# Performance work log

Measured on AMD Instinct MI355X. Metric: run time of the kernel, lower is better.

## Reference

```python
import jax, jax.numpy as jnp
import numpy as np

S, D, M, K, H = 4096, 768, 1024, 32, 8
DH = D // H  # 96
CTX = 10
EPS_LN = 1e-5
EPS_COS = 1e-8


def setup_inputs() -> dict:
    key = jax.random.key(0)
    ks = jax.random.split(key, 30)
    sc = 0.02
    n = lambda k, shp: jax.random.normal(k, shp, jnp.float32) * sc
    inp = {
        "text_embeddings": jax.random.normal(ks[0], (1, S, D), jnp.float32),
        "candidate_embeddings": jax.random.normal(ks[1], (M, K, D), jnp.float32),
        "mention_starts": jax.random.randint(ks[2], (M,), 0, S - 16),
        "span_lengths": jax.random.randint(ks[3], (M,), 0, 8),
        # relik_reader: Linear(2D->D), ReLU, Linear(D->1)
        "relik_w1": n(ks[4], (2 * D, D)), "relik_b1": jnp.zeros((D,), jnp.float32),
        "relik_w2": n(ks[5], (D, 1)), "relik_b2": jnp.zeros((1,), jnp.float32),
        # TransformerEncoderLayer (post-norm, relu, nhead=8, ffn=4D)
        "wq": n(ks[6], (D, D)), "bq": jnp.zeros((D,), jnp.float32),
        "wk": n(ks[7], (D, D)), "bk": jnp.zeros((D,), jnp.float32),
        "wv": n(ks[8], (D, D)), "bv": jnp.zeros((D,), jnp.float32),
        "wo": n(ks[9], (D, D)), "bo": jnp.zeros((D,), jnp.float32),
        "ln1_g": jnp.ones((D,), jnp.float32), "ln1_b": jnp.zeros((D,), jnp.float32),
        "ffn_w1": n(ks[10], (D, 4 * D)), "ffn_b1": jnp.zeros((4 * D,), jnp.float32),
        "ffn_w2": n(ks[11], (4 * D, D)), "ffn_b2": jnp.zeros((D,), jnp.float32),
        "ln2_g": jnp.ones((D,), jnp.float32), "ln2_b": jnp.zeros((D,), jnp.float32),
        # unirel_interaction: Linear(2D->D), ReLU, Linear(D->D)
        "uni_w1": n(ks[12], (2 * D, D)), "uni_b1": jnp.zeros((D,), jnp.float32),
        "uni_w2": n(ks[13], (D, D)), "uni_b2": jnp.zeros((D,), jnp.float32),
    }
    return inp


def _ln(x, g, b):
    mu = jnp.mean(x, -1, keepdims=True)
    var = jnp.mean(jnp.square(x - mu), -1, keepdims=True)
    return (x - mu) * jax.lax.rsqrt(var + EPS_LN) * g + b


def reference(text_embeddings, candidate_embeddings, mention_starts, span_lengths,
              relik_w1, relik_b1, relik_w2, relik_b2,
              wq, bq, wk, bk, wv, bv, wo, bo,
              ln1_g, ln1_b, ffn_w1, ffn_b1, ffn_w2, ffn_b2, ln2_g, ln2_b,
              uni_w1, uni_b1, uni_w2, uni_b2):
    txt = text_embeddings[0]                               # [S, D]
    seq = txt.shape[0]
    csum = jnp.concatenate([jnp.zeros((1, txt.shape[1]), txt.dtype),
                            jnp.cumsum(txt, axis=0)], axis=0)  # [S+1, D]
    ends = mention_starts + span_lengths
    # mean over [start, end] inclusive
    m_len = (span_lengths + 1).astype(txt.dtype)
    mention = (csum[ends + 1] - csum[mention_starts]) / m_len[:, None]  # [M, D]
    # context mean over [c_start, c_end) exclusive, as in original slicing
    c_start = jnp.maximum(0, mention_starts - CTX)
    c_end = jnp.minimum(seq - 1, ends + CTX)
    ctx = (csum[c_end] - csum[c_start]) / (c_end - c_start).astype(txt.dtype)[:, None]

    cand = candidate_embeddings                            # [M, K, D]
    mk = jnp.broadcast_to(mention[:, None, :], cand.shape) # [M, K, D]

    # relik score: MLP on [mention; candidate]
    cat_mc = jnp.concatenate([mk, cand], axis=-1)          # [M, K, 2D]
    h = jax.nn.relu(cat_mc @ relik_w1 + relik_b1)
    relik = (h @ relik_w2 + relik_b2)[..., 0]              # [M, K]

    # 2-token transformer encoder layer over stack([mention, candidate])
    x = jnp.stack([mk, cand], axis=2)                      # [M, K, 2, D]
    q = (x @ wq + bq).reshape(M, K, 2, H, DH)
    k_ = (x @ wk + bk).reshape(M, K, 2, H, DH)
    v = (x @ wv + bv).reshape(M, K, 2, H, DH)
    scores = jnp.einsum("mkqhd,mkvhd->mkhqv", q, k_) / jnp.sqrt(jnp.float32(DH))
    attn = jax.nn.softmax(scores, axis=-1)
    o = jnp.einsum("mkhqv,mkvhd->mkqhd", attn, v).reshape(M, K, 2, D)
    x1 = _ln(x + (o @ wo + bo), ln1_g, ln1_b)
    f = jax.nn.relu(x1 @ ffn_w1 + ffn_b1) @ ffn_w2 + ffn_b2
    x2 = _ln(x1 + f, ln2_g, ln2_b)                         # [M, K, 2, D]
    e0, e1 = x2[..., 0, :], x2[..., 1, :]
    n0 = jnp.maximum(jnp.linalg.norm(e0, axis=-1), EPS_COS)
    n1 = jnp.maximum(jnp.linalg.norm(e1, axis=-1), EPS_COS)
    atg = jnp.sum(e0 * e1, axis=-1) / (n0 * n1)            # [M, K]

    # unirel: MLP on [context; candidate], sigmoid of mean
    ck = jnp.broadcast_to(ctx[:, None, :], cand.shape)
    cat_cc = jnp.concatenate([ck, cand], axis=-1)
    inter = jax.nn.relu(cat_cc @ uni_w1 + uni_b1) @ uni_w2 + uni_b2
    unirel = jax.nn.sigmoid(jnp.mean(inter, axis=-1))      # [M, K]

    return jnp.stack([relik, atg, unirel], axis=0)         # [3, M, K]
```

## Files before the change

### kernel.cpp

```cpp
#include <hip/hip_runtime.h>
#include <math.h>

#define S_LEN 4096
#define D_DIM 768
#define M_CNT 1024
#define K_CNT 32
#define MK_CNT 32768
#define DH_DIM 96
#define CTX_W 10

typedef __bf16 bf16_t;
typedef bf16_t bf16x8 __attribute__((ext_vector_type(8)));
typedef float f32x4 __attribute__((ext_vector_type(4)));
typedef float f32x16 __attribute__((ext_vector_type(16)));
typedef int i32x4 __attribute__((ext_vector_type(4)));
typedef int i32x8 __attribute__((ext_vector_type(8)));

__device__ __forceinline__ float block_reduce_sum(float v, float* sbuf) {
#pragma unroll
    for (int off = 32; off; off >>= 1) v += __shfl_down(v, off);
    __syncthreads();
    int wave = threadIdx.x >> 6;
    int lane = threadIdx.x & 63;
    if (lane == 0) sbuf[wave] = v;
    __syncthreads();
    return sbuf[0] + sbuf[1] + sbuf[2] + sbuf[3];
}

__device__ __forceinline__ float wave_sum(float v) {
#pragma unroll
    for (int off = 32; off; off >>= 1) v += __shfl_down(v, off);
    return __shfl(v, 0);
}

__device__ __forceinline__ unsigned char to_fp8(float v) {
    return (unsigned char)(__builtin_amdgcn_cvt_pk_fp8_f32(v, v, 0, false) & 0xff);
}

__device__ __forceinline__ void ld2(const bf16_t* p, float& a, float& b) {
    ushort2 u = *(const ushort2*)p;
    a = __uint_as_float((unsigned)u.x << 16);
    b = __uint_as_float((unsigned)u.y << 16);
}

template<int OUT_BF16, int RELU>
__global__ __launch_bounds__(256, 2) void gemm_mfma(
    const bf16_t* __restrict__ A, const bf16_t* __restrict__ Bt,
    const float* __restrict__ bias, void* __restrict__ C,
    int Kd, int N, int nx, int ny)
{
    __shared__ bf16_t As[128 * 64];
    __shared__ bf16_t Bs[128 * 64];
    const int tid = threadIdx.x;
    const int w = tid >> 6, l = tid & 63;
    int per = 8 * nx;
    int g = blockIdx.x / per, rr = blockIdx.x % per;
    int gs = ny - g * 8; if (gs > 8) gs = 8;
    const int row0 = (g * 8 + rr % gs) * 128, col0 = (rr / gs) * 128;

    const int srow = w * 8 + (l >> 3);
    const int gchunk = (l & 7) ^ ((l >> 3) & 7);
    const bf16_t* gA = A + (size_t)(row0 + srow) * Kd + gchunk * 8;
    const bf16_t* gB = Bt + (size_t)(col0 + srow) * Kd + gchunk * 8;

    const int wm = w >> 1, wn = w & 1;
    f32x4 acc[4][4] = {};

    for (int k0 = 0; k0 < Kd; k0 += 64) {
#pragma unroll
        for (int c = 0; c < 4; ++c) {
            __builtin_amdgcn_global_load_lds(
                (const __attribute__((address_space(1))) void*)(gA + (size_t)(c * 32) * Kd + k0),
                (__attribute__((address_space(3))) void*)(As + (c * 256 + w * 64) * 8), 16, 0, 0);
            __builtin_amdgcn_global_load_lds(
                (const __attribute__((address_space(1))) void*)(gB + (size_t)(c * 32) * Kd + k0),
                (__attribute__((address_space(3))) void*)(Bs + (c * 256 + w * 64) * 8), 16, 0, 0);
        }
        __syncthreads();
#pragma unroll
        for (int ks = 0; ks < 2; ++ks) {
            bf16x8 af[4], bfr[4];
#pragma unroll
            for (int i = 0; i < 4; ++i) {
                int arow = wm * 64 + i * 16 + (l & 15);
                int slot = (ks * 4 + (l >> 4)) ^ (l & 7);
                af[i] = *(const bf16x8*)(As + arow * 64 + slot * 8);
                int brow = wn * 64 + i * 16 + (l & 15);
                bfr[i] = *(const bf16x8*)(Bs + brow * 64 + slot * 8);
            }
#pragma unroll
            for (int i = 0; i < 4; ++i)
#pragma unroll
                for (int j = 0; j < 4; ++j)
                    acc[i][j] = __builtin_amdgcn_mfma_f32_16x16x32_bf16(af[i], bfr[j], acc[i][j], 0, 0, 0);
        }
        __syncthreads();
    }

#pragma unroll
    for (int i = 0; i < 4; ++i) {
        int row = row0 + wm * 64 + i * 16 + (l >> 4) * 4;
#pragma unroll
        for (int j = 0; j < 4; ++j) {
            int col = col0 + wn * 64 + j * 16 + (l & 15);
            float bv = bias ? bias[col] : 0.f;
#pragma unroll
            for (int r = 0; r < 4; ++r) {
                float v = acc[i][j][r] + bv;
                if (RELU) v = fmaxf(v, 0.f);
                if (OUT_BF16) ((bf16_t*)C)[(size_t)(row + r) * N + col] = (bf16_t)v;
                else          ((float*)C)[(size_t)(row + r) * N + col] = v;
            }
        }
    }
}

static inline void launch_gemm(const bf16_t* A, const bf16_t* Bt, const float* bias, void* C,
                               int rows, int Kd, int N, bool relu, bool outbf, hipStream_t st) {
    int nx = N / 128, ny = rows / 128;
    dim3 grid(nx * ny);
    if (outbf) {
        if (relu) gemm_mfma<1, 1><<<grid, 256, 0, st>>>(A, Bt, bias, C, Kd, N, nx, ny);
        else      gemm_mfma<1, 0><<<grid, 256, 0, st>>>(A, Bt, bias, C, Kd, N, nx, ny);
    } else {
        if (relu) gemm_mfma<0, 1><<<grid, 256, 0, st>>>(A, Bt, bias, C, Kd, N, nx, ny);
        else      gemm_mfma<0, 0><<<grid, 256, 0, st>>>(A, Bt, bias, C, Kd, N, nx, ny);
    }
}

template<int OMODE, int RELU, int RESID>
__global__ __launch_bounds__(256, 2) void gemm_fp8(
    const unsigned char* __restrict__ A, const unsigned char* __restrict__ Bp,
    const float* __restrict__ bias, void* __restrict__ C,
    const bf16_t* __restrict__ resid,
    int Kd, int N, int nx, int ny)
{
    __shared__ unsigned char As[256 * 128];
    const int tid = threadIdx.x;
    const int w = tid >> 6, l = tid & 63;
    int per = 8 * nx;
    int g = blockIdx.x / per, rrb = blockIdx.x % per;
    int gs = ny - g * 8; if (gs > 8) gs = 8;
    const int row0 = (g * 8 + rrb % gs) * 256, col0 = (rrb / gs) * 128;
    const int wm = w >> 1, wn = w & 1;
    const int SA = 0x7F7F7F7F;
    const int KT = Kd >> 7;

    const int srow = w * 8 + (l >> 3);
    const int gch = (l & 7) ^ ((l >> 3) & 7);
    const unsigned char* gA = A + (size_t)(row0 + srow) * Kd + gch * 16;

    const int cg0 = (col0 >> 5) + wn * 2;
    const unsigned char* gB0 = Bp + (size_t)cg0 * KT * 4096 + (l >> 5) * 1024 + (l & 31) * 16;
    const unsigned char* gB1 = gB0 + (size_t)KT * 4096;

    f32x16 acc[4][2] = {};

    for (int kt = 0; kt < KT; ++kt) {
#pragma unroll
        for (int q = 0; q < 8; ++q)
            __builtin_amdgcn_global_load_lds(
                (const __attribute__((address_space(1))) void*)(gA + (size_t)(q * 32) * Kd + kt * 128),
                (__attribute__((address_space(3))) void*)(As + (q * 256 + w * 64) * 16), 16, 0, 0);

        const unsigned char* p0 = gB0 + (size_t)kt * 4096;
        const unsigned char* p1 = gB1 + (size_t)kt * 4096;
        i32x4 b00l = *(const i32x4*)(p0);
        i32x4 b00h = *(const i32x4*)(p0 + 512);
        i32x4 b01l = *(const i32x4*)(p0 + 2048);
        i32x4 b01h = *(const i32x4*)(p0 + 2560);
        i32x4 b10l = *(const i32x4*)(p1);
        i32x4 b10h = *(const i32x4*)(p1 + 512);
        i32x4 b11l = *(const i32x4*)(p1 + 2048);
        i32x4 b11h = *(const i32x4*)(p1 + 2560);

        __syncthreads();

#pragma unroll
        for (int s = 0; s < 2; ++s) {
            int cb = s * 4 + ((l >> 5) << 1);
            i32x8 af[4], bfr[2];
#pragma unroll
            for (int i = 0; i < 4; ++i) {
                int row = wm * 128 + i * 32 + (l & 31);
                int sl0 = cb ^ (row & 7);
                int sl1 = (cb + 1) ^ (row & 7);
                i32x4 lo = *(const i32x4*)(As + (row * 8 + sl0) * 16);
                i32x4 hi = *(const i32x4*)(As + (row * 8 + sl1) * 16);
                i32x8 a;
                a[0] = lo[0]; a[1] = lo[1]; a[2] = lo[2]; a[3] = lo[3];
                a[4] = hi[0]; a[5] = hi[1]; a[6] = hi[2]; a[7] = hi[3];
                af[i] = a;
            }
            {
                i32x4 lo = s ? b01l : b00l;
                i32x4 hi = s ? b01h : b00h;
                i32x8 b;
                b[0] = lo[0]; b[1] = lo[1]; b[2] = lo[2]; b[3] = lo[3];
                b[4] = hi[0]; b[5] = hi[1]; b[6] = hi[2]; b[7] = hi[3];
                bfr[0] = b;
                lo = s ? b11l : b10l;
                hi = s ? b11h : b10h;
                b[0] = lo[0]; b[1] = lo[1]; b[2] = lo[2]; b[3] = lo[3];
                b[4] = hi[0]; b[5] = hi[1]; b[6] = hi[2]; b[7] = hi[3];
                bfr[1] = b;
            }
#pragma unroll
            for (int i = 0; i < 4; ++i)
#pragma unroll
                for (int j = 0; j < 2; ++j)
                    acc[i][j] = __builtin_amdgcn_mfma_scale_f32_32x32x64_f8f6f4(
                        af[i], bfr[j], acc[i][j], 0, 0, 0, SA, 0, SA);
        }
        __syncthreads();
    }

#pragma unroll
    for (int i = 0; i < 4; ++i) {
        int rbase = row0 + wm * 128 + i * 32 + 4 * (l >> 5);
#pragma unroll
        for (int j = 0; j < 2; ++j) {
            int col = col0 + wn * 64 + j * 32 + (l & 31);
            float bv = bias ? bias[col] : 0.f;
#pragma unroll
            for (int reg = 0; reg < 16; ++reg) {
                int row = rbase + (reg & 3) + 8 * (reg >> 2);
                float v = acc[i][j][reg] + bv;
                if (RESID) v += (float)resid[(size_t)row * N + col];
                if (RELU) v = fmaxf(v, 0.f);
                if (OMODE == 1)
                    ((unsigned char*)C)[(size_t)row * N + col] = to_fp8(v);
                else if (OMODE == 2)
                    ((bf16_t*)C)[(size_t)row * N + col] = (bf16_t)v;
                else
                    ((float*)C)[(size_t)row * N + col] = v;
            }
        }
    }
}

template<int OMODE, int RELU, int RESID>
static inline void launch_fp8_t(const unsigned char* A, const unsigned char* Bp, const float* bias,
                                void* C, const bf16_t* resid, int rows, int Kd, int N, hipStream_t st) {
    int nx = N / 128, ny = rows / 256;
    gemm_fp8<OMODE, RELU, RESID><<<dim3(nx * ny), 256, 0, st>>>(A, Bp, bias, C, resid, Kd, N, nx, ny);
}

__global__ __launch_bounds__(256) void transpose_bf16(
    const float* __restrict__ W, bf16_t* __restrict__ Wt, int Kd, int N)
{
    __shared__ float t[32][33];
    int bx = blockIdx.x * 32, by = blockIdx.y * 32;
    int x = threadIdx.x & 31, y = threadIdx.x >> 5;
#pragma unroll
    for (int yy = y; yy < 32; yy += 8) t[yy][x] = W[(size_t)(by + yy) * N + bx + x];
    __syncthreads();
#pragma unroll
    for (int yy = y; yy < 32; yy += 8) Wt[(size_t)(bx + yy) * Kd + by + x] = (bf16_t)t[x][yy];
}

__global__ __launch_bounds__(256) void pack_fp8(
    const float* __restrict__ W, unsigned char* __restrict__ P, int Kd, int N)
{
    __shared__ float t[32][33];
    int bx = blockIdx.x * 32, by = blockIdx.y * 32;
    int x = threadIdx.x & 31, y = threadIdx.x >> 5;
#pragma unroll
    for (int yy = y; yy < 32; yy += 8) t[yy][x] = W[(size_t)(by + yy) * N + bx + x];
    __syncthreads();
    int xg = threadIdx.x & 7, yo = threadIdx.x >> 3;
    int lo = __builtin_amdgcn_cvt_pk_fp8_f32(t[xg * 4 + 0][yo], t[xg * 4 + 1][yo], 0, false);
    int both = __builtin_amdgcn_cvt_pk_fp8_f32(t[xg * 4 + 2][yo], t[xg * 4 + 3][yo], lo, true);
    int cg = blockIdx.x;
    int kt = by >> 7;
    int s = (by >> 6) & 1;
    int half = (by >> 5) & 1;
    int chunk = xg >> 2;
    size_t off = (((size_t)cg * (Kd >> 7) + kt) * 4096) + s * 2048 + half * 1024
               + chunk * 512 + yo * 16 + (xg & 3) * 4;
    *(int*)(P + off) = both;
}

__global__ __launch_bounds__(256) void cvt_cand(
    const float* __restrict__ x, bf16_t* __restrict__ yb,
    unsigned char* __restrict__ yq, int n4)
{
    int i = blockIdx.x * 256 + threadIdx.x;
    if (i < n4) {
        float4 v = ((const float4*)x)[i];
        bf16_t o4[4] = {(bf16_t)v.x, (bf16_t)v.y, (bf16_t)v.z, (bf16_t)v.w};
        ((uint2*)yb)[i] = *(uint2*)o4;
        int lo = __builtin_amdgcn_cvt_pk_fp8_f32(v.x, v.y, 0, false);
        int both = __builtin_amdgcn_cvt_pk_fp8_f32(v.z, v.w, lo, true);
        ((int*)yq)[i] = both;
    }
}

__global__ __launch_bounds__(256) void pack_bias(
    const float* __restrict__ bq, const float* __restrict__ bk,
    const float* __restrict__ bv, float* __restrict__ o)
{
    int i = blockIdx.x * 256 + threadIdx.x;
    if (i < 768) { o[i] = bq[i]; o[i + 768] = bk[i]; o[i + 1536] = bv[i]; }
}

__global__ __launch_bounds__(256) void spans_kernel(
    const float* __restrict__ txt, const int* __restrict__ starts,
    const int* __restrict__ lens, float* __restrict__ mention,
    unsigned char* __restrict__ mentionq, bf16_t* __restrict__ mentionb,
    bf16_t* __restrict__ ctxb)
{
    int m = blockIdx.x;
    int st = starts[m], ln = lens[m];
    int en = st + ln;
    int cs = st - CTX_W; if (cs < 0) cs = 0;
    int ce = en + CTX_W; if (ce > S_LEN - 1) ce = S_LEN - 1;
    int c = threadIdx.x;
    float s0 = 0.f, s1 = 0.f, s2 = 0.f;
    for (int r = st; r <= en; ++r) {
        const float* tr = txt + (size_t)r * D_DIM;
        s0 += tr[c]; s1 += tr[c + 256]; s2 += tr[c + 512];
    }
    float inv = 1.f / (float)(ln + 1);
    float v0 = s0 * inv, v1 = s1 * inv, v2 = s2 * inv;
    float* mp = mention + (size_t)m * D_DIM;
    bf16_t* mb = mentionb + (size_t)m * D_DIM;
    unsigned char* mq = mentionq + (size_t)m * D_DIM;
    mp[c] = v0; mp[c + 256] = v1; mp[c + 512] = v2;
    mb[c] = (bf16_t)v0; mb[c + 256] = (bf16_t)v1; mb[c + 512] = (bf16_t)v2;
    mq[c] = to_fp8(v0); mq[c + 256] = to_fp8(v1); mq[c + 512] = to_fp8(v2);

    s0 = 0.f; s1 = 0.f; s2 = 0.f;
    for (int r = cs; r < ce; ++r) {
        const float* tr = txt + (size_t)r * D_DIM;
        s0 += tr[c]; s1 += tr[c + 256]; s2 += tr[c + 512];
    }
    inv = 1.f / (float)(ce - cs);
    bf16_t* cp = ctxb + (size_t)m * D_DIM;
    cp[c] = (bf16_t)(s0 * inv); cp[c + 256] = (bf16_t)(s1 * inv); cp[c + 512] = (bf16_t)(s2 * inv);
}

__global__ __launch_bounds__(256) void w2bar_kernel(
    const float* __restrict__ uni_w2, const float* __restrict__ uni_b2,
    float* __restrict__ w2bar, float* __restrict__ b2bar)
{
    __shared__ float sbuf[4];
    int d = blockIdx.x;
    float s = 0.f;
    if (d < D_DIM) {
        for (int j = threadIdx.x; j < D_DIM; j += 256) s += uni_w2[(size_t)d * D_DIM + j];
        s = block_reduce_sum(s, sbuf);
        if (threadIdx.x == 0) w2bar[d] = s * (1.f / (float)D_DIM);
    } else {
        for (int j = threadIdx.x; j < D_DIM; j += 256) s += uni_b2[j];
        s = block_reduce_sum(s, sbuf);
        if (threadIdx.x == 0) *b2bar = s * (1.f / (float)D_DIM);
    }
}

__global__ __launch_bounds__(512) void attn_kernel(
    const bf16_t* __restrict__ qkvm, const bf16_t* __restrict__ qkvc,
    unsigned char* __restrict__ o, int g0)
{
    int lc = blockIdx.x;
    int gg = g0 + lc;
    int m = gg >> 5;
    int h = threadIdx.x >> 6;
    int lane = threadIdx.x & 63;
    const bf16_t* bm = qkvm + (size_t)m * 2304 + h * DH_DIM;
    const bf16_t* bc = qkvc + (size_t)lc * 2304 + h * DH_DIM;

    float s00 = 0.f, s01 = 0.f, s10 = 0.f, s11 = 0.f;
    int d = lane * 2;
    if (lane < 48) {
        float qm0, qm1, km0, km1, qc0, qc1, kc0, kc1;
        ld2(bm + d, qm0, qm1);
        ld2(bm + 768 + d, km0, km1);
        ld2(bc + d, qc0, qc1);
        ld2(bc + 768 + d, kc0, kc1);
        s00 = qm0 * km0 + qm1 * km1;
        s01 = qm0 * kc0 + qm1 * kc1;
        s10 = qc0 * km0 + qc1 * km1;
        s11 = qc0 * kc0 + qc1 * kc1;
    }
#pragma unroll
    for (int off = 32; off; off >>= 1) {
        s00 += __shfl_down(s00, off); s01 += __shfl_down(s01, off);
        s10 += __shfl_down(s10, off); s11 += __shfl_down(s11, off);
    }
    s00 = __shfl(s00, 0); s01 = __shfl(s01, 0);
    s10 = __shfl(s10, 0); s11 = __shfl(s11, 0);
    const float sc = 0.1020620726159658f;
    s00 *= sc; s01 *= sc; s10 *= sc; s11 *= sc;
    float m0 = fmaxf(s00, s01), m1 = fmaxf(s10, s11);
    float e00 = expf(s00 - m0), e01 = expf(s01 - m0);
    float e10 = expf(s10 - m1), e11 = expf(s11 - m1);
    float i0 = 1.f / (e00 + e01), i1 = 1.f / (e10 + e11);
    float a00 = e00 * i0, a01 = e01 * i0, a10 = e10 * i1, a11 = e11 * i1;

    unsigned char* o0 = o + ((size_t)lc * 2) * D_DIM + h * DH_DIM;
    unsigned char* o1 = o0 + D_DIM;
    if (lane < 48) {
        float vm0, vm1, vc0, vc1;
        ld2(bm + 1536 + d, vm0, vm1);
        ld2(bc + 1536 + d, vc0, vc1);
        unsigned r0 = __builtin_amdgcn_cvt_pk_fp8_f32(a00 * vm0 + a01 * vc0, a00 * vm1 + a01 * vc1, 0, false);
        unsigned r1 = __builtin_amdgcn_cvt_pk_fp8_f32(a10 * vm0 + a11 * vc0, a10 * vm1 + a11 * vc1, 0, false);
        *(unsigned short*)(o0 + d) = (unsigned short)(r0 & 0xffff);
        *(unsigned short*)(o1 + d) = (unsigned short)(r1 & 0xffff);
    }
}

__global__ __launch_bounds__(256) void ln1_kernel(
    const bf16_t* __restrict__ x1pre, const float* __restrict__ mention,
    const bf16_t* __restrict__ candb, const float* __restrict__ g,
    const float* __restrict__ b, bf16_t* __restrict__ x1f,
    unsigned char* __restrict__ x1q, int g0)
{
    int w = threadIdx.x >> 6, l = threadIdx.x & 63;
    int r = blockIdx.x * 4 + w;
    int lc = r >> 1, pos = r & 1;
    int gg = g0 + lc, m = gg >> 5;
    float v[12];
    const bf16_t* pr = x1pre + (size_t)r * D_DIM;
    if (pos) {
        const bf16_t* xr = candb + (size_t)gg * D_DIM;
#pragma unroll
        for (int i = 0; i < 12; ++i) { int j = l + i * 64; v[i] = (float)xr[j] + (float)pr[j]; }
    } else {
        const float* xr = mention + (size_t)m * D_DIM;
#pragma unroll
        for (int i = 0; i < 12; ++i) { int j = l + i * 64; v[i] = xr[j] + (float)pr[j]; }
    }
    float s = 0.f;
#pragma unroll
    for (int i = 0; i < 12; ++i) s += v[i];
    float mu = wave_sum(s) * (1.f / (float)D_DIM);
    float vv = 0.f;
#pragma unroll
    for (int i = 0; i < 12; ++i) { float d = v[i] - mu; vv += d * d; }
    float var = wave_sum(vv) * (1.f / (float)D_DIM);
    float inv = rsqrtf(var + 1e-5f);
    bf16_t* fp = x1f + (size_t)r * D_DIM;
    unsigned char* qp = x1q + (size_t)r * D_DIM;
#pragma unroll
    for (int i = 0; i < 12; ++i) {
        int j = l + i * 64;
        float o = (v[i] - mu) * inv * g[j] + b[j];
        fp[j] = (bf16_t)o;
        qp[j] = to_fp8(o);
    }
}

__global__ __launch_bounds__(256) void heads_kernel(
    const bf16_t* __restrict__ y,
    const float* __restrict__ g2, const float* __restrict__ b2g,
    const float* __restrict__ Ar, const float* __restrict__ Au,
    const bf16_t* __restrict__ ru, const float* __restrict__ rw2,
    const float* __restrict__ rb2, const float* __restrict__ w2bar,
    const float* __restrict__ b2bar, float* __restrict__ out, int g0)
{
    int w = threadIdx.x >> 6, l = threadIdx.x & 63;
    int lc = blockIdx.x * 4 + w;
    int gg = g0 + lc, m = gg >> 5;
    const bf16_t* y0 = y + (size_t)(2 * lc) * D_DIM;
    const bf16_t* y1 = y0 + D_DIM;
    float v0[12], v1[12];
    float s0 = 0.f, s1 = 0.f;
#pragma unroll
    for (int i = 0; i < 12; ++i) {
        int j = l + i * 64;
        v0[i] = (float)y0[j]; v1[i] = (float)y1[j];
        s0 += v0[i]; s1 += v1[i];
    }
    float mu0 = wave_sum(s0) * (1.f / (float)D_DIM);
    float mu1 = wave_sum(s1) * (1.f / (float)D_DIM);
    float q0 = 0.f, q1 = 0.f;
#pragma unroll
    for (int i = 0; i < 12; ++i) {
        float d0 = v0[i] - mu0, d1 = v1[i] - mu1;
        q0 += d0 * d0; q1 += d1 * d1;
    }
    float inv0 = rsqrtf(wave_sum(q0) * (1.f / (float)D_DIM) + 1e-5f);
    float inv1 = rsqrtf(wave_sum(q1) * (1.f / (float)D_DIM) + 1e-5f);

    const float* ar = Ar + (size_t)m * D_DIM;
    const float* au = Au + (size_t)m * D_DIM;
    const bf16_t* br = ru + (size_t)lc * 1536;
    const bf16_t* bu = br + 768;

    float dd = 0.f, aa = 0.f, bb = 0.f, rs = 0.f, us = 0.f;
#pragma unroll
    for (int i = 0; i < 12; ++i) {
        int j = l + i * 64;
        float e0 = (v0[i] - mu0) * inv0 * g2[j] + b2g[j];
        float e1 = (v1[i] - mu1) * inv1 * g2[j] + b2g[j];
        dd += e0 * e1; aa += e0 * e0; bb += e1 * e1;
        rs += fmaxf(ar[j] + (float)br[j], 0.f) * rw2[j];
        us += fmaxf(au[j] + (float)bu[j], 0.f) * w2bar[j];
    }
    dd = wave_sum(dd); aa = wave_sum(aa); bb = wave_sum(bb);
    rs = wave_sum(rs); us = wave_sum(us);
    if (l == 0) {
        float n0 = fmaxf(sqrtf(aa), 1e-8f);
        float n1 = fmaxf(sqrtf(bb), 1e-8f);
        out[MK_CNT + gg] = dd / (n0 * n1);
        out[gg] = rs + rb2[0];
        float z = us + *b2bar;
        out[2 * MK_CNT + gg] = 1.f / (1.f + expf(-z));
    }
}

extern "C" void kernel_launch(void* const* d_in, const int* in_sizes, int n_in,
                              void* d_out, int out_size, void* d_ws, size_t ws_size,
                              hipStream_t stream) {
    const float* text     = (const float*)d_in[0];
    const float* cand     = (const float*)d_in[1];
    const int*   starts   = (const int*)d_in[2];
    const int*   lens     = (const int*)d_in[3];
    const float* relik_w1 = (const float*)d_in[4];
    const float* relik_b1 = (const float*)d_in[5];
    const float* relik_w2 = (const float*)d_in[6];
    const float* relik_b2 = (const float*)d_in[7];
    const float* wq = (const float*)d_in[8];
    const float* bq = (const float*)d_in[9];
    const float* wk = (const float*)d_in[10];
    const float* bk = (const float*)d_in[11];
    const float* wv = (const float*)d_in[12];
    const float* bv = (const float*)d_in[13];
    const float* wo = (const float*)d_in[14];
    const float* bo = (const float*)d_in[15];
    const float* ln1_g = (const float*)d_in[16];
    const float* ln1_b = (const float*)d_in[17];
    const float* ffn_w1 = (const float*)d_in[18];
    const float* ffn_b1 = (const float*)d_in[19];
    const float* ffn_w2 = (const float*)d_in[20];
    const float* ffn_b2 = (const float*)d_in[21];
    const float* ln2_g = (const float*)d_in[22];
    const float* ln2_b = (const float*)d_in[23];
    const float* uni_w1 = (const float*)d_in[24];
    const float* uni_b1 = (const float*)d_in[25];
    const float* uni_w2 = (const float*)d_in[26];
    const float* uni_b2 = (const float*)d_in[27];
    float* out = (float*)d_out;

    const size_t MD = (size_t)M_CNT * D_DIM;
    const size_t DD = (size_t)D_DIM * D_DIM;

    size_t fixed_f = 26500000;
    int NC = 32768;
    while (NC > 256 && (fixed_f + (size_t)NC * 4224) * 4 > ws_size) NC >>= 1;
    const size_t NCD = (size_t)NC * D_DIM;

    float* p = (float*)d_ws;
    float* mention = p; p += MD;
    float* Ar      = p; p += MD;
    float* Au      = p; p += MD;
    float* bqkv    = p; p += 2304;
    float* w2bar   = p; p += 768;
    float* b2bar   = p; p += 64;
    bf16_t* mentionb = (bf16_t*)p; p += MD / 2;
    bf16_t* ctxb     = (bf16_t*)p; p += MD / 2;
    unsigned char* mentionq = (unsigned char*)p; p += MD / 4;
    bf16_t* qkvm     = (bf16_t*)p; p += (size_t)M_CNT * 2304 / 2;
    bf16_t* relikAT  = (bf16_t*)p; p += DD / 2;
    bf16_t* uniAT    = (bf16_t*)p; p += DD / 2;
    bf16_t* wruT     = (bf16_t*)p; p += 2 * DD / 2;
    unsigned char* wqkvq = (unsigned char*)p; p += 3 * DD / 4;
    unsigned char* woq   = (unsigned char*)p; p += DD / 4;
    unsigned char* w1q = (unsigned char*)p; p += (size_t)3072 * 768 / 4;
    unsigned char* w2q = (unsigned char*)p; p += (size_t)3072 * 768 / 4;
    bf16_t* candb    = (bf16_t*)p; p += (size_t)MK_CNT * D_DIM / 2;
    unsigned char* candq = (unsigned char*)p; p += (size_t)MK_CNT * D_DIM / 4;

    bf16_t* qkvcb = (bf16_t*)p;
    bf16_t* x1f   = (bf16_t*)p;
    unsigned char* x1q = (unsigned char*)(x1f + 2 * NCD);
    p += (size_t)NC * 2304 / 2;
    bf16_t* rucb  = (bf16_t*)p; p += (size_t)NC * 1536 / 2;
    bf16_t* x1pre = (bf16_t*)p;
    bf16_t* x2f   = x1pre;
    p += NCD;
    unsigned char* hb   = (unsigned char*)p;
    unsigned char* obuf = hb;
    p += (size_t)NC * 1536;

    dim3 t768(768 / 32, 768 / 32);
    pack_fp8<<<t768, 256, 0, stream>>>(wq, wqkvq, 768, 768);
    pack_fp8<<<t768, 256, 0, stream>>>(wk, wqkvq + DD, 768, 768);
    pack_fp8<<<t768, 256, 0, stream>>>(wv, wqkvq + 2 * DD, 768, 768);
    pack_fp8<<<t768, 256, 0, stream>>>(wo, woq, 768, 768);
    transpose_bf16<<<t768, 256, 0, stream>>>(relik_w1 + DD, wruT, 768, 768);
    transpose_bf16<<<t768, 256, 0, stream>>>(uni_w1 + DD, wruT + DD, 768, 768);
    transpose_bf16<<<t768, 256, 0, stream>>>(relik_w1, relikAT, 768, 768);
    transpose_bf16<<<t768, 256, 0, stream>>>(uni_w1, uniAT, 768, 768);
    pack_fp8<<<dim3(3072 / 32, 768 / 32), 256, 0, stream>>>(ffn_w1, w1q, 768, 3072);
    pack_fp8<<<dim3(768 / 32, 3072 / 32), 256, 0, stream>>>(ffn_w2, w2q, 3072, 768);
    pack_bias<<<3, 256, 0, stream>>>(bq, bk, bv, bqkv);
    w2bar_kernel<<<D_DIM + 1, 256, 0, stream>>>(uni_w2, uni_b2, w2bar, b2bar);
    cvt_cand<<<(MK_CNT * D_DIM / 4 + 255) / 256, 256, 0, stream>>>(cand, candb, candq, MK_CNT * D_DIM / 4);

    spans_kernel<<<M_CNT, 256, 0, stream>>>(text, starts, lens, mention, mentionq, mentionb, ctxb);
    launch_fp8_t<2, 0, 0>(mentionq, wqkvq, bqkv, qkvm, nullptr, M_CNT, 768, 2304, stream);
    launch_gemm(mentionb, relikAT, relik_b1, Ar, M_CNT, 768, 768, false, false, stream);
    launch_gemm(ctxb, uniAT, uni_b1, Au, M_CNT, 768, 768, false, false, stream);

    int nch = MK_CNT / NC;
    for (int c = 0; c < nch; ++c) {
        int g0 = c * NC;
        launch_fp8_t<2, 0, 0>(candq + (size_t)g0 * D_DIM, wqkvq, bqkv, qkvcb, nullptr, NC, 768, 2304, stream);
        launch_gemm(candb + (size_t)g0 * D_DIM, wruT, nullptr, rucb, NC, 768, 1536, false, true, stream);

        attn_kernel<<<NC, 512, 0, stream>>>(qkvm, qkvcb, obuf, g0);

        launch_fp8_t<2, 0, 0>(obuf, woq, bo, x1pre, nullptr, 2 * NC, 768, 768, stream);
        ln1_kernel<<<2 * NC / 4, 256, 0, stream>>>(x1pre, mention, candb,
                                                   ln1_g, ln1_b, x1f, x1q, g0);

        launch_fp8_t<1, 1, 0>(x1q, w1q, ffn_b1, hb, nullptr, 2 * NC, 768, 3072, stream);
        launch_fp8_t<2, 0, 1>(hb, w2q, ffn_b2, x2f, x1f, 2 * NC, 3072, 768, stream);

        heads_kernel<<<NC / 4, 256, 0, stream>>>(x2f, ln2_g, ln2_b, Ar, Au, rucb,
                                                 relik_w2, relik_b2, w2bar, b2bar, out, g0);
    }
}
```

Measured before the change: 1.186 ms.

## Pipeline FP8 GEMM with 4-stage LDS ring, 256x256 tiles and 512 threads

Rewrites the FP8 MFMA GEMM main loop. A is staged through a 4-buffer LDS ring with prefetch two k-tiles ahead, and B fragments are register double-buffered one tile ahead. The output tile grows to 256x256 with 8 waves per block, and s_setprio plus sched_barrier interleave loads with MFMAs. The goal is to hide global-load latency and reuse A across more columns. The cost is 128KB of LDS per block, which limits occupancy, and N must now be a multiple of 256.

```diff
diff --git a/kernel.cpp b/kernel.cpp
--- a/kernel.cpp
+++ b/kernel.cpp
@@ -129,91 +129,95 @@
 }
 
 template<int OMODE, int RELU, int RESID>
-__global__ __launch_bounds__(256, 2) void gemm_fp8(
+__global__ __launch_bounds__(512, 2) void gemm_fp8(
     const unsigned char* __restrict__ A, const unsigned char* __restrict__ Bp,
     const float* __restrict__ bias, void* __restrict__ C,
     const bf16_t* __restrict__ resid,
     int Kd, int N, int nx, int ny)
 {
-    __shared__ unsigned char As[256 * 128];
+    __shared__ unsigned char As[4 * 256 * 128];
     const int tid = threadIdx.x;
     const int w = tid >> 6, l = tid & 63;
     int per = 8 * nx;
     int g = blockIdx.x / per, rrb = blockIdx.x % per;
     int gs = ny - g * 8; if (gs > 8) gs = 8;
-    const int row0 = (g * 8 + rrb % gs) * 256, col0 = (rrb / gs) * 128;
-    const int wm = w >> 1, wn = w & 1;
+    const int row0 = (g * 8 + rrb % gs) * 256, col0 = (rrb / gs) * 256;
+    const int wm = w >> 2, wn = w & 3;
     const int SA = 0x7F7F7F7F;
     const int KT = Kd >> 7;
 
-    const int srow = w * 8 + (l >> 3);
-    const int gch = (l & 7) ^ ((l >> 3) & 7);
-    const unsigned char* gA = A + (size_t)(row0 + srow) * Kd + gch * 16;
+    const int gch = (tid & 7) ^ ((tid >> 3) & 7);
+    const unsigned char* gA = A + (size_t)(row0 + (tid >> 3)) * Kd + gch * 16;
 
     const int cg0 = (col0 >> 5) + wn * 2;
     const unsigned char* gB0 = Bp + (size_t)cg0 * KT * 4096 + (l >> 5) * 1024 + (l & 31) * 16;
     const unsigned char* gB1 = gB0 + (size_t)KT * 4096;
 
     f32x16 acc[4][2] = {};
-
-    for (int kt = 0; kt < KT; ++kt) {
-#pragma unroll
-        for (int q = 0; q < 8; ++q)
-            __builtin_amdgcn_global_load_lds(
-                (const __attribute__((address_space(1))) void*)(gA + (size_t)(q * 32) * Kd + kt * 128),
-                (__attribute__((address_space(3))) void*)(As + (q * 256 + w * 64) * 16), 16, 0, 0);
-
-        const unsigned char* p0 = gB0 + (size_t)kt * 4096;
-        const unsigned char* p1 = gB1 + (size_t)kt * 4096;
-        i32x4 b00l = *(const i32x4*)(p0);
-        i32x4 b00h = *(const i32x4*)(p0 + 512);
-        i32x4 b01l = *(const i32x4*)(p0 + 2048);
-        i32x4 b01h = *(const i32x4*)(p0 + 2560);
-        i32x4 b10l = *(const i32x4*)(p1);
-        i32x4 b10h = *(const i32x4*)(p1 + 512);
-        i32x4 b11l = *(const i32x4*)(p1 + 2048);
-        i32x4 b11h = *(const i32x4*)(p1 + 2560);
-
-        __syncthreads();
-
-#pragma unroll
-        for (int s = 0; s < 2; ++s) {
-            int cb = s * 4 + ((l >> 5) << 1);
-            i32x8 af[4], bfr[2];
-#pragma unroll
-            for (int i = 0; i < 4; ++i) {
-                int row = wm * 128 + i * 32 + (l & 31);
-                int sl0 = cb ^ (row & 7);
-                int sl1 = (cb + 1) ^ (row & 7);
-                i32x4 lo = *(const i32x4*)(As + (row * 8 + sl0) * 16);
-                i32x4 hi = *(const i32x4*)(As + (row * 8 + sl1) * 16);
-                i32x8 a;
-                a[0] = lo[0]; a[1] = lo[1]; a[2] = lo[2]; a[3] = lo[3];
-                a[4] = hi[0]; a[5] = hi[1]; a[6] = hi[2]; a[7] = hi[3];
-                af[i] = a;
-            }
-            {
-                i32x4 lo = s ? b01l : b00l;
-                i32x4 hi = s ? b01h : b00h;
-                i32x8 b;
-                b[0] = lo[0]; b[1] = lo[1]; b[2] = lo[2]; b[3] = lo[3];
-                b[4] = hi[0]; b[5] = hi[1]; b[6] = hi[2]; b[7] = hi[3];
-                bfr[0] = b;
-                lo = s ? b11l : b10l;
-                hi = s ? b11h : b10h;
-                b[0] = lo[0]; b[1] = lo[1]; b[2] = lo[2]; b[3] = lo[3];
-                b[4] = hi[0]; b[5] = hi[1]; b[6] = hi[2]; b[7] = hi[3];
-                bfr[1] = b;
-            }
-#pragma unroll
-            for (int i = 0; i < 4; ++i)
-#pragma unroll
-                for (int j = 0; j < 2; ++j)
-                    acc[i][j] = __builtin_amdgcn_mfma_scale_f32_32x32x64_f8f6f4(
-                        af[i], bfr[j], acc[i][j], 0, 0, 0, SA, 0, SA);
-        }
-        __syncthreads();
-    }
+    i32x8 bA0, bA1, bA2, bA3, bB0, bB1, bB2, bB3;
+
+    auto stageA = [&](int buf, int ktv, int c) {
+        __builtin_amdgcn_global_load_lds(
+            (const __attribute__((address_space(1))) void*)(gA + (size_t)(c * 64) * Kd + ktv * 128),
+            (__attribute__((address_space(3))) void*)(As + buf * 32768 + c * 8192 + w * 1024), 16, 0, 0);
+    };
+
+#define LOADB8(b0v, b1v, b2v, b3v, ktv)                                         \
+    {   const unsigned char* p0_ = gB0 + (size_t)(ktv) * 4096;                  \
+        const unsigned char* p1_ = gB1 + (size_t)(ktv) * 4096;                  \
+        i32x4 q0 = *(const i32x4*)(p0_),        q1 = *(const i32x4*)(p0_ + 512);\
+        i32x4 q2 = *(const i32x4*)(p0_ + 2048), q3 = *(const i32x4*)(p0_ + 2560);\
+        i32x4 q4 = *(const i32x4*)(p1_),        q5 = *(const i32x4*)(p1_ + 512);\
+        i32x4 q6 = *(const i32x4*)(p1_ + 2048), q7 = *(const i32x4*)(p1_ + 2560);\
+        b0v = (i32x8){q0[0],q0[1],q0[2],q0[3],q1[0],q1[1],q1[2],q1[3]};         \
+        b1v = (i32x8){q2[0],q2[1],q2[2],q2[3],q3[0],q3[1],q3[2],q3[3]};         \
+        b2v = (i32x8){q4[0],q4[1],q4[2],q4[3],q5[0],q5[1],q5[2],q5[3]};         \
+        b3v = (i32x8){q6[0],q6[1],q6[2],q6[3],q7[0],q7[1],q7[2],q7[3]};         }
+
+#define KT_STEP(T, BU0, BU1, BU2, BU3, BP0, BP1, BP2, BP3, DO_PRE, DO_STAGE, VMS) \
+    {   asm volatile("s_waitcnt vmcnt(" VMS ")" ::: "memory");                  \
+        __builtin_amdgcn_s_barrier();                                           \
+        __builtin_amdgcn_sched_barrier(0);                                      \
+        const unsigned char* as_ = As + ((T) & 3) * 32768;                      \
+        _Pragma("unroll")                                                       \
+        for (int p = 0; p < 4; ++p) {                                           \
+            if (p == 0 && (DO_PRE)) LOADB8(BP0, BP1, BP2, BP3, (T) + 1);        \
+            if (DO_STAGE) stageA(((T) + 2) & 3, (T) + 2, p);                    \
+            int row_ = wm * 128 + p * 32 + (l & 31);                            \
+            int c0_ = (l >> 5) << 1;                                            \
+            i32x4 a0l = *(const i32x4*)(as_ + row_ * 128 + (((c0_    )) ^ (row_ & 7)) * 16); \
+            i32x4 a0h = *(const i32x4*)(as_ + row_ * 128 + (((c0_ + 1)) ^ (row_ & 7)) * 16); \
+            i32x4 a1l = *(const i32x4*)(as_ + row_ * 128 + (((c0_ + 4)) ^ (row_ & 7)) * 16); \
+            i32x4 a1h = *(const i32x4*)(as_ + row_ * 128 + (((c0_ + 5)) ^ (row_ & 7)) * 16); \
+            __builtin_amdgcn_s_barrier();                                       \
+            __builtin_amdgcn_sched_barrier(0);                                  \
+            i32x8 af0 = (i32x8){a0l[0],a0l[1],a0l[2],a0l[3],a0h[0],a0h[1],a0h[2],a0h[3]}; \
+            i32x8 af1 = (i32x8){a1l[0],a1l[1],a1l[2],a1l[3],a1h[0],a1h[1],a1h[2],a1h[3]}; \
+            __builtin_amdgcn_s_setprio(1);                                      \
+            acc[p][0] = __builtin_amdgcn_mfma_scale_f32_32x32x64_f8f6f4(af0, BU0, acc[p][0], 0, 0, 0, SA, 0, SA); \
+            acc[p][0] = __builtin_amdgcn_mfma_scale_f32_32x32x64_f8f6f4(af1, BU1, acc[p][0], 0, 0, 0, SA, 0, SA); \
+            acc[p][1] = __builtin_amdgcn_mfma_scale_f32_32x32x64_f8f6f4(af0, BU2, acc[p][1], 0, 0, 0, SA, 0, SA); \
+            acc[p][1] = __builtin_amdgcn_mfma_scale_f32_32x32x64_f8f6f4(af1, BU3, acc[p][1], 0, 0, 0, SA, 0, SA); \
+            __builtin_amdgcn_s_setprio(0);                                      \
+            __builtin_amdgcn_sched_barrier(0);                                  \
+        }                                                                       }
+
+    LOADB8(bA0, bA1, bA2, bA3, 0);
+#pragma unroll
+    for (int c = 0; c < 4; ++c) stageA(0, 0, c);
+#pragma unroll
+    for (int c = 0; c < 4; ++c) stageA(1, 1, c);
+
+    int t = 0;
+    for (; t + 2 < KT; t += 2) {
+        KT_STEP(t,     bA0,bA1,bA2,bA3, bB0,bB1,bB2,bB3, 1, 1, "4");
+        KT_STEP(t + 1, bB0,bB1,bB2,bB3, bA0,bA1,bA2,bA3, 1, (t + 3) < KT, "4");
+    }
+    KT_STEP(KT - 2, bA0,bA1,bA2,bA3, bB0,bB1,bB2,bB3, 1, 0, "4");
+    KT_STEP(KT - 1, bB0,bB1,bB2,bB3, bA0,bA1,bA2,bA3, 0, 0, "0");
+
+#undef KT_STEP
+#undef LOADB8
 
 #pragma unroll
     for (int i = 0; i < 4; ++i) {
@@ -242,8 +246,8 @@
 template<int OMODE, int RELU, int RESID>
 static inline void launch_fp8_t(const unsigned char* A, const unsigned char* Bp, const float* bias,
                                 void* C, const bf16_t* resid, int rows, int Kd, int N, hipStream_t st) {
-    int nx = N / 128, ny = rows / 256;
-    gemm_fp8<OMODE, RELU, RESID><<<dim3(nx * ny), 256, 0, st>>>(A, Bp, bias, C, resid, Kd, N, nx, ny);
+    int nx = N / 256, ny = rows / 256;
+    gemm_fp8<OMODE, RELU, RESID><<<dim3(nx * ny), 512, 0, st>>>(A, Bp, bias, C, resid, Kd, N, nx, ny);
 }
 
 __global__ __launch_bounds__(256) void transpose_bf16(
```

New measurement: 3.577 ms. +201.7%, slower.
